# Performance work log

Hardware: AMD Instinct MI355X
Metric: run time of the kernel (lower is better)

Reference implementation:

```python
import jax, jax.numpy as jnp
import numpy as np

DIM = 128
NUM_HEADS = 8
HEAD_DIM = DIM // NUM_HEADS
N_NODES = 50000
N_EDGES = 800000


def setup_inputs() -> dict:
    key = jax.random.key(0)
    ks = jax.random.split(key, 10)
    scale = 1.0 / np.sqrt(DIM)
    x = jax.random.normal(ks[0], (N_NODES, DIM), dtype=jnp.float32)
    edge_index = jax.random.randint(ks[1], (2, N_EDGES), 0, N_NODES, dtype=jnp.int64)
    Wq = jax.random.normal(ks[2], (DIM, DIM), dtype=jnp.float32) * scale
    bq = jnp.zeros((DIM,), dtype=jnp.float32)
    Wk = jax.random.normal(ks[3], (DIM, DIM), dtype=jnp.float32) * scale
    bk = jnp.zeros((DIM,), dtype=jnp.float32)
    Wv = jax.random.normal(ks[4], (DIM, DIM), dtype=jnp.float32) * scale
    bv = jnp.zeros((DIM,), dtype=jnp.float32)
    Wo = jax.random.normal(ks[5], (DIM, DIM), dtype=jnp.float32) * scale
    bo = jnp.zeros((DIM,), dtype=jnp.float32)
    return {"x": x, "edge_index": edge_index, "Wq": Wq, "bq": bq,
            "Wk": Wk, "bk": bk, "Wv": Wv, "bv": bv, "Wo": Wo, "bo": bo}


def reference(x, edge_index, Wq, bq, Wk, bk, Wv, bv, Wo, bo):
    n = x.shape[0]
    tgt = edge_index[0]  # softmax group / scatter destination
    src = edge_index[1]  # gather source
    # projections: torch nn.Linear -> x @ W.T + b
    q = (x @ Wq.T + bq).reshape(n, NUM_HEADS, HEAD_DIM)
    k = (x @ Wk.T + bk).reshape(n, NUM_HEADS, HEAD_DIM)
    v = (x @ Wv.T + bv).reshape(n, NUM_HEADS, HEAD_DIM)
    # edge-wise attention scores: [E, H]
    scores = jnp.einsum('ehd,ehd->eh', q[src], k[tgt]) / np.sqrt(HEAD_DIM).astype(np.float32)
    # segment softmax over edges grouped by target node
    m = jax.ops.segment_max(scores, tgt, num_segments=n)          # [N, H]
    m = jax.lax.stop_gradient(m)
    p = jnp.exp(scores - m[tgt])                                   # [E, H]
    s = jax.ops.segment_sum(p, tgt, num_segments=n)               # [N, H]
    probs = p / s[tgt]
    # weighted scatter-add of source values
    weighted = v[src] * probs[..., None]                           # [E, H, D]
    agg = jax.ops.segment_sum(weighted, tgt, num_segments=n)      # [N, H, D]
    out = agg.reshape(n, DIM) @ Wo.T + bo
    # dropout is identity in eval mode
    return out
```

## Files before the change

kernel.cpp:

```cpp
#include <hip/hip_runtime.h>
#include <math.h>

#define NN 50000
#define NE 800000
#define DIM 128
#define NH 8
#define HD 16
#define NTILE 3125
#define TPB 782
#define LROW 136
#define QVROW 256
#define SCAN_B 196

typedef short v8s __attribute__((ext_vector_type(8)));
typedef float v4f __attribute__((ext_vector_type(4)));

__device__ __forceinline__ unsigned short f2b(float f) {
    unsigned u = __float_as_uint(f);
    u = (u + 0x7fffu + ((u >> 16) & 1u)) >> 16;
    return (unsigned short)u;
}
__device__ __forceinline__ float blo(unsigned w) { return __uint_as_float(w << 16); }
__device__ __forceinline__ float bhi(unsigned w) { return __uint_as_float(w & 0xffff0000u); }

template<int PAT>
__device__ __forceinline__ float swz(float x) {
    return __int_as_float(__builtin_amdgcn_ds_swizzle(__float_as_int(x), PAT));
}

#define NW4 (4 * DIM * DIM / 4)
#define NC4 ((NN + 3) / 4)
__global__ __launch_bounds__(256) void convert_kernel(
    const float* __restrict__ Wq, const float* __restrict__ Wk,
    const float* __restrict__ Wv, const float* __restrict__ Wo,
    unsigned short* __restrict__ Wb, int* __restrict__ cnt)
{
    int i = blockIdx.x * 256 + threadIdx.x;
    if (i < NW4) {
        int mat = i >> 12;
        int off = i & 4095;
        const float* Wsrc = (mat == 0) ? Wq : (mat == 1) ? Wk : (mat == 2) ? Wv : Wo;
        float4 f = ((const float4*)Wsrc)[off];
        uint2 o;
        o.x = (unsigned)f2b(f.x) | ((unsigned)f2b(f.y) << 16);
        o.y = (unsigned)f2b(f.z) | ((unsigned)f2b(f.w) << 16);
        ((uint2*)(Wb + (size_t)mat * DIM * DIM))[off] = o;
    } else if (i < NW4 + NC4) {
        ((int4*)cnt)[i - NW4] = make_int4(0, 0, 0, 0);
    }
}

__global__ __launch_bounds__(256) void qkv_mfma_kernel(
    const float* __restrict__ x, const unsigned short* __restrict__ Wb,
    const float* __restrict__ bq, const float* __restrict__ bk, const float* __restrict__ bv,
    unsigned short* __restrict__ qvb, unsigned short* __restrict__ kb,
    const int* __restrict__ tgt, int* __restrict__ cnt)
{
    __shared__ unsigned short Wl[DIM * LROW];
    const int tid = threadIdx.x;
    const int lane = tid & 63;
    const int warp = tid >> 6;
    const int m = lane & 15;
    const int quad = lane >> 4;

    const int gsize = TPB * 256;
    for (int e = blockIdx.x * 256 + tid; e < NE; e += gsize)
        atomicAdd(cnt + tgt[e], 1);

    const int rt = blockIdx.x * 4 + warp;
    const int r0 = rt * 16;
    const bool act = (rt < NTILE);

    v8s a[4];
    if (act) {
#pragma unroll
        for (int kt = 0; kt < 4; ++kt) {
            const float4* xr = (const float4*)(x + (size_t)(r0 + m) * DIM + kt * 32 + quad * 8);
            float4 f0 = xr[0], f1 = xr[1];
            v8s t;
            t[0] = (short)f2b(f0.x); t[1] = (short)f2b(f0.y);
            t[2] = (short)f2b(f0.z); t[3] = (short)f2b(f0.w);
            t[4] = (short)f2b(f1.x); t[5] = (short)f2b(f1.y);
            t[6] = (short)f2b(f1.z); t[7] = (short)f2b(f1.w);
            a[kt] = t;
        }
    }

#pragma unroll
    for (int mat = 0; mat < 3; ++mat) {
        if (mat) __syncthreads();
        const unsigned short* Wg = Wb + (size_t)mat * DIM * DIM;
#pragma unroll
        for (int it = 0; it < 8; ++it) {
            int chunk = it * 256 + tid;
            int row = chunk >> 4, c8 = chunk & 15;
            *(uint4*)(Wl + row * LROW + c8 * 8) = ((const uint4*)Wg)[chunk];
        }
        __syncthreads();

        if (act) {
            const float* bias_p = (mat == 0) ? bq : (mat == 1) ? bk : bv;
#pragma unroll
            for (int nt = 0; nt < 8; ++nt) {
                v4f c = {0.f, 0.f, 0.f, 0.f};
#pragma unroll
                for (int kt = 0; kt < 4; ++kt) {
                    v8s b = *(const v8s*)(Wl + (nt * 16 + m) * LROW + kt * 32 + quad * 8);
                    c = __builtin_amdgcn_mfma_f32_16x16x32_bf16(a[kt], b, c, 0, 0, 0);
                }
                int col = nt * 16 + m;
                float bias = bias_p[col];
#pragma unroll
                for (int i = 0; i < 4; ++i) {
                    int row = r0 + quad * 4 + i;
                    unsigned short val = f2b(c[i] + bias);
                    if (mat == 1) {
                        kb[(size_t)row * DIM + col] = val;
                    } else {
                        int pos = (col >> 1) * 4 + (col & 1) + ((mat == 2) ? 2 : 0);
                        qvb[(size_t)row * QVROW + pos] = val;
                    }
                }
            }
        }
    }
}

__global__ __launch_bounds__(256) void scan1_kernel(
    const int* __restrict__ cnt, int* __restrict__ off, int* __restrict__ bsum)
{
    __shared__ int ws4[4];
    const int tid = threadIdx.x, lane = tid & 63, wid = tid >> 6;
    int i = blockIdx.x * 256 + tid;
    int v0 = (i < NN) ? cnt[i] : 0;
    int incl = v0;
#pragma unroll
    for (int d = 1; d < 64; d <<= 1) {
        int t = __shfl_up(incl, d);
        if (lane >= d) incl += t;
    }
    if (lane == 63) ws4[wid] = incl;
    __syncthreads();
    int wexcl = 0;
#pragma unroll
    for (int t = 0; t < 3; ++t) if (t < wid) wexcl += ws4[t];
    if (i < NN) off[i] = wexcl + incl - v0;
    if (tid == 255) bsum[blockIdx.x] = wexcl + incl;
}

__global__ __launch_bounds__(256) void scan23_kernel(
    const int* __restrict__ bsum, int* __restrict__ off, int* __restrict__ cursor)
{
    __shared__ int ws4[4];
    __shared__ int base_s, total_s;
    const int tid = threadIdx.x, lane = tid & 63, wid = tid >> 6;
    int v0 = (tid < SCAN_B) ? bsum[tid] : 0;
    int incl = v0;
#pragma unroll
    for (int d = 1; d < 64; d <<= 1) {
        int t = __shfl_up(incl, d);
        if (lane >= d) incl += t;
    }
    if (lane == 63) ws4[wid] = incl;
    __syncthreads();
    int wexcl = 0;
#pragma unroll
    for (int t = 0; t < 3; ++t) if (t < wid) wexcl += ws4[t];
    int excl = wexcl + incl - v0;
    if (tid == blockIdx.x) base_s = excl;
    if (tid == SCAN_B - 1) total_s = excl + v0;
    __syncthreads();
    int i = blockIdx.x * 256 + tid;
    if (i < NN) {
        int t = off[i] + base_s;
        off[i] = t;
        cursor[i] = t;
    }
    if (blockIdx.x == SCAN_B - 1 && tid == 0) off[NN] = total_s;
}

__global__ __launch_bounds__(256) void fill_kernel(
    const int* __restrict__ tgt, const int* __restrict__ src,
    int* __restrict__ cursor, int* __restrict__ edge_src)
{
    int e = blockIdx.x * 256 + threadIdx.x;
    if (e >= NE) return;
    int t = tgt[e];
    int pos = atomicAdd(cursor + t, 1);
    edge_src[pos] = src[e];
}

__global__ __launch_bounds__(256) void attn_kernel(
    const int* __restrict__ off, const int* __restrict__ edge_src,
    const unsigned short* __restrict__ qvb, const unsigned short* __restrict__ kb,
    unsigned short* __restrict__ aggb)
{
    const int tid = threadIdx.x;
    const int lane = tid & 63;
    const int node = blockIdx.x * 4 + (tid >> 6);
    if (node >= NN) return;

    const int base = __builtin_amdgcn_readfirstlane(off[node]);
    const int deg  = __builtin_amdgcn_readfirstlane(off[node + 1]) - base;

    unsigned kw = *(const unsigned*)(kb + (size_t)node * DIM + 2 * lane);
    const float klo = blo(kw), khi = bhi(kw);
    const int j = lane & 7;

    float ax = 0.f, ay = 0.f, ss = 0.f;

    for (int c0 = 0; c0 < deg; c0 += 64) {
        const int nchunk = min(deg - c0, 64);
        int srcv = edge_src[base + c0 + min(lane, nchunk - 1)];
        for (int b = 0; b < nchunk; b += 8) {
            const int nb = min(nchunk - b, 8);
            uint2 qv[8];
#pragma unroll
            for (int i = 0; i < 8; ++i) {
                int si = __builtin_amdgcn_readlane(srcv, min(b + i, nchunk - 1));
                qv[i] = ((const uint2*)(qvb + (size_t)si * QVROW))[lane];
            }
            float part[8];
#pragma unroll
            for (int i = 0; i < 8; ++i)
                part[i] = blo(qv[i].x) * klo + bhi(qv[i].x) * khi;
            float r1[4];
#pragma unroll
            for (int t = 0; t < 4; ++t) {
                float keep = (j & 1) ? part[2 * t + 1] : part[2 * t];
                float send = (j & 1) ? part[2 * t]     : part[2 * t + 1];
                r1[t] = keep + swz<0x041F>(send);
            }
            float r2[2];
#pragma unroll
            for (int u = 0; u < 2; ++u) {
                float keep = (j & 2) ? r1[2 * u + 1] : r1[2 * u];
                float send = (j & 2) ? r1[2 * u]     : r1[2 * u + 1];
                r2[u] = keep + swz<0x081F>(send);
            }
            float keep = (j & 4) ? r2[1] : r2[0];
            float send = (j & 4) ? r2[0] : r2[1];
            float tot = keep + swz<0x101F>(send);
            float p = (j < nb) ? __expf(tot * 0.25f) : 0.f;
            ss += p;
#define ACC(i) { float pi = swz<((i) << 5) | 0x18>(p); unsigned vv = qv[i].y; \
                 ax += pi * blo(vv); ay += pi * bhi(vv); }
            ACC(0) ACC(1) ACC(2) ACC(3) ACC(4) ACC(5) ACC(6) ACC(7)
#undef ACC
        }
    }
    ss += swz<0x041F>(ss);
    ss += swz<0x081F>(ss);
    ss += swz<0x101F>(ss);

    unsigned* ap = (unsigned*)(aggb + (size_t)node * DIM + 2 * lane);
    if (deg == 0) {
        *ap = 0u;
    } else {
        float inv = 1.f / ss;
        *ap = (unsigned)f2b(ax * inv) | ((unsigned)f2b(ay * inv) << 16);
    }
}

__global__ __launch_bounds__(256) void outproj_mfma_kernel(
    const unsigned short* __restrict__ aggb, const unsigned short* __restrict__ Wob,
    const float* __restrict__ bo, float* __restrict__ out)
{
    __shared__ unsigned short Wl[DIM * LROW];
    const int tid = threadIdx.x;
    const int lane = tid & 63;
    const int warp = tid >> 6;
    const int m = lane & 15;
    const int quad = lane >> 4;

#pragma unroll
    for (int it = 0; it < 8; ++it) {
        int chunk = it * 256 + tid;
        int row = chunk >> 4, c8 = chunk & 15;
        *(uint4*)(Wl + row * LROW + c8 * 8) = ((const uint4*)Wob)[chunk];
    }
    __syncthreads();

    const int rt = blockIdx.x * 4 + warp;
    if (rt >= NTILE) return;
    const int r0 = rt * 16;

    v8s a[4];
#pragma unroll
    for (int kt = 0; kt < 4; ++kt)
        a[kt] = *(const v8s*)(aggb + (size_t)(r0 + m) * DIM + kt * 32 + quad * 8);

#pragma unroll
    for (int nt = 0; nt < 8; ++nt) {
        v4f c = {0.f, 0.f, 0.f, 0.f};
#pragma unroll
        for (int kt = 0; kt < 4; ++kt) {
            v8s b = *(const v8s*)(Wl + (nt * 16 + m) * LROW + kt * 32 + quad * 8);
            c = __builtin_amdgcn_mfma_f32_16x16x32_bf16(a[kt], b, c, 0, 0, 0);
        }
        int col = nt * 16 + m;
        float bias = bo[col];
#pragma unroll
        for (int i = 0; i < 4; ++i) {
            int row = r0 + quad * 4 + i;
            out[(size_t)row * DIM + col] = c[i] + bias;
        }
    }
}

extern "C" void kernel_launch(void* const* d_in, const int* in_sizes, int n_in,
                              void* d_out, int out_size, void* d_ws, size_t ws_size,
                              hipStream_t stream) {
    const float* x  = (const float*)d_in[0];
    const int*   ei = (const int*)d_in[1];
    const float* Wq = (const float*)d_in[2];
    const float* bq = (const float*)d_in[3];
    const float* Wk = (const float*)d_in[4];
    const float* bk = (const float*)d_in[5];
    const float* Wv = (const float*)d_in[6];
    const float* bv = (const float*)d_in[7];
    const float* Wo = (const float*)d_in[8];
    const float* bo = (const float*)d_in[9];

    const int* tgt = ei;
    const int* src = ei + NE;

    char* ws = (char*)d_ws;
    const size_t SZ_QV = (size_t)NN * QVROW * 2;
    const size_t SZ_BF = (size_t)NN * DIM * 2;

    unsigned short* qvb  = (unsigned short*)(ws);
    unsigned short* kb   = (unsigned short*)(ws + SZ_QV);
    unsigned short* aggb = (unsigned short*)(ws + SZ_QV + SZ_BF);
    unsigned short* Wb   = (unsigned short*)(ws + SZ_QV + 2 * SZ_BF);

    char* wi = ws + SZ_QV + 2 * SZ_BF + (size_t)4 * DIM * DIM * 2;
    int* cnt      = (int*)(wi);
    int* off      = (int*)(wi + (size_t)NN * 4);
    int* cursor   = (int*)(wi + (size_t)(2 * NN + 1) * 4);
    int* edge_src = (int*)(wi + (size_t)(3 * NN + 1) * 4);
    int* bsum     = (int*)(wi + (size_t)(3 * NN + 1) * 4 + (size_t)NE * 4);

    const int conv_blocks = (NW4 + NC4 + 255) / 256;
    const int edge_blocks = (NE + 255) / 256;

    convert_kernel<<<conv_blocks, 256, 0, stream>>>(Wq, Wk, Wv, Wo, Wb, cnt);
    qkv_mfma_kernel<<<TPB, 256, 0, stream>>>(x, Wb, bq, bk, bv, qvb, kb, tgt, cnt);
    scan1_kernel<<<SCAN_B, 256, 0, stream>>>(cnt, off, bsum);
    scan23_kernel<<<SCAN_B, 256, 0, stream>>>(bsum, off, cursor);
    fill_kernel<<<edge_blocks, 256, 0, stream>>>(tgt, src, cursor, edge_src);
    attn_kernel<<<(NN + 3) / 4, 256, 0, stream>>>(off, edge_src, qvb, kb, aggb);
    outproj_mfma_kernel<<<TPB, 256, 0, stream>>>(
        aggb, Wb + (size_t)3 * DIM * DIM, bo, (float*)d_out);
}
```

Before: 253.1 us.

## Split QKV projection across per-matrix blocks and pack bf16 output stores

Launches three times as many blocks so each block computes only one of the Q/K/V projections, removing the per-block sequence of three weight reloads and the barriers between them. The x tile is now read and converted to bf16 three times instead of once. Output stores are also widened: neighbouring lanes exchange values through ds_swizzle so each lane writes a 32-bit pair of bf16 values instead of 16-bit scalars. The edge-count atomics are spread over the larger grid.

```diff
diff --git a/kernel.cpp b/kernel.cpp
--- a/kernel.cpp
+++ b/kernel.cpp
@@ -57,71 +57,76 @@
     const int* __restrict__ tgt, int* __restrict__ cnt)
 {
     __shared__ unsigned short Wl[DIM * LROW];
+    const int mat = blockIdx.x / TPB;
+    const int tg  = blockIdx.x % TPB;
     const int tid = threadIdx.x;
     const int lane = tid & 63;
     const int warp = tid >> 6;
     const int m = lane & 15;
     const int quad = lane >> 4;
 
-    const int gsize = TPB * 256;
+    const int gsize = 3 * TPB * 256;
     for (int e = blockIdx.x * 256 + tid; e < NE; e += gsize)
         atomicAdd(cnt + tgt[e], 1);
 
-    const int rt = blockIdx.x * 4 + warp;
+    const unsigned short* Wg = Wb + (size_t)mat * DIM * DIM;
+#pragma unroll
+    for (int it = 0; it < 8; ++it) {
+        int chunk = it * 256 + tid;
+        int row = chunk >> 4, c8 = chunk & 15;
+        *(uint4*)(Wl + row * LROW + c8 * 8) = ((const uint4*)Wg)[chunk];
+    }
+    __syncthreads();
+
+    const int rt = tg * 4 + warp;
+    if (rt >= NTILE) return;
     const int r0 = rt * 16;
-    const bool act = (rt < NTILE);
+
+    const float* bias_p = (mat == 0) ? bq : (mat == 1) ? bk : bv;
 
     v8s a[4];
-    if (act) {
+#pragma unroll
+    for (int kt = 0; kt < 4; ++kt) {
+        const float4* xr = (const float4*)(x + (size_t)(r0 + m) * DIM + kt * 32 + quad * 8);
+        float4 f0 = xr[0], f1 = xr[1];
+        v8s t;
+        t[0] = (short)f2b(f0.x); t[1] = (short)f2b(f0.y);
+        t[2] = (short)f2b(f0.z); t[3] = (short)f2b(f0.w);
+        t[4] = (short)f2b(f1.x); t[5] = (short)f2b(f1.y);
+        t[6] = (short)f2b(f1.z); t[7] = (short)f2b(f1.w);
+        a[kt] = t;
+    }
+
+    const int i0 = (lane & 1) ? 2 : 0;
+
+#pragma unroll
+    for (int nt = 0; nt < 8; ++nt) {
+        v4f c = {0.f, 0.f, 0.f, 0.f};
 #pragma unroll
         for (int kt = 0; kt < 4; ++kt) {
-            const float4* xr = (const float4*)(x + (size_t)(r0 + m) * DIM + kt * 32 + quad * 8);
-            float4 f0 = xr[0], f1 = xr[1];
-            v8s t;
-            t[0] = (short)f2b(f0.x); t[1] = (short)f2b(f0.y);
-            t[2] = (short)f2b(f0.z); t[3] = (short)f2b(f0.w);
-            t[4] = (short)f2b(f1.x); t[5] = (short)f2b(f1.y);
-            t[6] = (short)f2b(f1.z); t[7] = (short)f2b(f1.w);
-            a[kt] = t;
-        }
-    }
-
-#pragma unroll
-    for (int mat = 0; mat < 3; ++mat) {
-        if (mat) __syncthreads();
-        const unsigned short* Wg = Wb + (size_t)mat * DIM * DIM;
-#pragma unroll
-        for (int it = 0; it < 8; ++it) {
-            int chunk = it * 256 + tid;
-            int row = chunk >> 4, c8 = chunk & 15;
-            *(uint4*)(Wl + row * LROW + c8 * 8) = ((const uint4*)Wg)[chunk];
-        }
-        __syncthreads();
-
-        if (act) {
-            const float* bias_p = (mat == 0) ? bq : (mat == 1) ? bk : bv;
-#pragma unroll
-            for (int nt = 0; nt < 8; ++nt) {
-                v4f c = {0.f, 0.f, 0.f, 0.f};
-#pragma unroll
-                for (int kt = 0; kt < 4; ++kt) {
-                    v8s b = *(const v8s*)(Wl + (nt * 16 + m) * LROW + kt * 32 + quad * 8);
-                    c = __builtin_amdgcn_mfma_f32_16x16x32_bf16(a[kt], b, c, 0, 0, 0);
-                }
-                int col = nt * 16 + m;
-                float bias = bias_p[col];
-#pragma unroll
-                for (int i = 0; i < 4; ++i) {
-                    int row = r0 + quad * 4 + i;
-                    unsigned short val = f2b(c[i] + bias);
-                    if (mat == 1) {
-                        kb[(size_t)row * DIM + col] = val;
-                    } else {
-                        int pos = (col >> 1) * 4 + (col & 1) + ((mat == 2) ? 2 : 0);
-                        qvb[(size_t)row * QVROW + pos] = val;
-                    }
-                }
-            }
+            v8s b = *(const v8s*)(Wl + (nt * 16 + m) * LROW + kt * 32 + quad * 8);
+            c = __builtin_amdgcn_mfma_f32_16x16x32_bf16(a[kt], b, c, 0, 0, 0);
+        }
+        int col = nt * 16 + m;
+        float bias = bias_p[col];
+        unsigned w0 = 0, w1 = 0;
+#pragma unroll
+        for (int i = 0; i < 4; ++i) {
+            unsigned own  = (unsigned)f2b(c[i] + bias);
+            unsigned part = (unsigned)__builtin_amdgcn_ds_swizzle((int)own, 0x041F) & 0xffffu;
+            unsigned w = (lane & 1) ? (part | (own << 16)) : (own | (part << 16));
+            if (i == i0)     w0 = w;
+            if (i == i0 + 1) w1 = w;
+        }
+        int colb = nt * 16 + (m & ~1);
+        int rowa = r0 + quad * 4 + i0;
+        if (mat == 1) {
+            *(unsigned*)(kb + (size_t)rowa * DIM + colb)       = w0;
+            *(unsigned*)(kb + (size_t)(rowa + 1) * DIM + colb) = w1;
+        } else {
+            int pos = colb * 2 + ((mat == 2) ? 2 : 0);
+            *(unsigned*)(qvb + (size_t)rowa * QVROW + pos)       = w0;
+            *(unsigned*)(qvb + (size_t)(rowa + 1) * QVROW + pos) = w1;
         }
     }
 }
@@ -345,7 +350,7 @@
     const int edge_blocks = (NE + 255) / 256;
 
     convert_kernel<<<conv_blocks, 256, 0, stream>>>(Wq, Wk, Wv, Wo, Wb, cnt);
-    qkv_mfma_kernel<<<TPB, 256, 0, stream>>>(x, Wb, bq, bk, bv, qvb, kb, tgt, cnt);
+    qkv_mfma_kernel<<<3 * TPB, 256, 0, stream>>>(x, Wb, bq, bk, bv, qvb, kb, tgt, cnt);
     scan1_kernel<<<SCAN_B, 256, 0, stream>>>(cnt, off, bsum);
     scan23_kernel<<<SCAN_B, 256, 0, stream>>>(bsum, off, cursor);
     fill_kernel<<<edge_blocks, 256, 0, stream>>>(tgt, src, cursor, edge_src);
```

Result: no change. 248.4 us (-1.9%).
